# Kernel tuning notes

Measured on AMD Instinct MI355X. Metric: run time of the kernel, lower is better.

The kernel has to match this reference:

```python
import jax, jax.numpy as jnp
import numpy as np
import math

B, T, D = 4, 2048, 1024
H, KD, VD = 16, 64, 64


def setup_inputs() -> dict:
    key = jax.random.key(0)
    ks = jax.random.split(key, 10)
    s = 1.0 / math.sqrt(D)
    x = jax.random.normal(ks[0], (B, T, D), dtype=jnp.float32)
    # causal mask: True above the diagonal (positions to be masked out)
    mask = jnp.triu(jnp.ones((1, T, T), dtype=bool), k=1)
    Wq = jax.random.normal(ks[1], (H * KD, D), dtype=jnp.float32) * s
    bq = jnp.zeros((H * KD,), dtype=jnp.float32)
    Wk = jax.random.normal(ks[2], (H * KD, D), dtype=jnp.float32) * s
    bk = jnp.zeros((H * KD,), dtype=jnp.float32)
    Wv = jax.random.normal(ks[3], (H * VD, D), dtype=jnp.float32) * s
    bv = jnp.zeros((H * VD,), dtype=jnp.float32)
    Wo = jax.random.normal(ks[4], (D, H * VD), dtype=jnp.float32) * (1.0 / math.sqrt(H * VD))
    bo = jnp.zeros((D,), dtype=jnp.float32)
    return {"x": x, "mask": mask, "Wq": Wq, "bq": bq, "Wk": Wk, "bk": bk,
            "Wv": Wv, "bv": bv, "Wo": Wo, "bo": bo}


def reference(x, mask, Wq, bq, Wk, bk, Wv, bv, Wo, bo):
    b, t, d = x.shape
    # projections, reshaped to (b, h, t, head_dim)
    q = (x @ Wq.T + bq).reshape(b, t, H, KD).transpose(0, 2, 1, 3)
    k = (x @ Wk.T + bk).reshape(b, t, H, KD).transpose(0, 2, 1, 3)
    v = (x @ Wv.T + bv).reshape(b, t, H, VD).transpose(0, 2, 1, 3)
    scores = jnp.einsum('bhqd,bhkd->bhqk', q, k) / jnp.sqrt(jnp.float32(KD))
    # mask [1,T,T] broadcasts over batch and heads
    scores = jnp.where(mask[:, None, :, :], -jnp.inf, scores)
    attn = jax.nn.softmax(scores, axis=-1)
    out = jnp.einsum('bhqk,bhkd->bhqd', attn, v)  # (b,h,t,vd)
    out = out.transpose(0, 2, 1, 3).reshape(b, t, H * VD)
    return out @ Wo.T + bo
```

## Files before the change

### kernel.cpp

```cpp
#include <hip/hip_runtime.h>
#include <hip/hip_bf16.h>
#include <stdint.h>

#define B_ 4
#define T_ 2048
#define D_ 1024
#define H_ 16
#define HD_ 64

typedef __attribute__((ext_vector_type(8))) short bf16x8;
typedef __attribute__((ext_vector_type(4))) float f32x4;
typedef __attribute__((ext_vector_type(16))) float f32x16;

static __device__ __forceinline__ short f2bf(float f) {
    __hip_bfloat16 h = __float2bfloat16(f);
    short s;
    __builtin_memcpy(&s, &h, sizeof(short));
    return s;
}
static __device__ __forceinline__ float bf2f(short s) {
    unsigned u = ((unsigned)(unsigned short)s) << 16;
    float f;
    __builtin_memcpy(&f, &u, sizeof(float));
    return f;
}

static __device__ __forceinline__ void gload16(const void* g, void* l) {
    __builtin_amdgcn_global_load_lds((const __attribute__((address_space(1))) uint32_t*)g,
                                     (__attribute__((address_space(3))) uint32_t*)l,
                                     16, 0, 0);
}

static __device__ __forceinline__ unsigned cvtpk(float lo, float hi) {
    unsigned r;
    asm("v_cvt_pk_bf16_f32 %0, %1, %2" : "=v"(r) : "v"(lo), "v"(hi));
    return r;
}
static __device__ __forceinline__ void pl32swap(unsigned& a, unsigned& b) {
    asm("v_permlane32_swap_b32 %0, %1" : "+v"(a), "+v"(b));
}

__global__ __launch_bounds__(256) void cast_kernel(const float* __restrict__ src,
                                                   short* __restrict__ dst, int n) {
    int i = (blockIdx.x * 256 + threadIdx.x) * 4;
    if (i < n) {
        float4 v = *reinterpret_cast<const float4*>(src + i);
        short4 o;
        o.x = f2bf(v.x); o.y = f2bf(v.y); o.z = f2bf(v.z); o.w = f2bf(v.w);
        *reinterpret_cast<short4*>(dst + i) = o;
    }
}

__global__ __launch_bounds__(256) void cast_w_kernel(const float* __restrict__ wq,
                                                     const float* __restrict__ wk,
                                                     const float* __restrict__ wv,
                                                     const float* __restrict__ wo,
                                                     short* __restrict__ wqkv,
                                                     short* __restrict__ wob) {
    int wsel = blockIdx.x >> 10;
    int blk = blockIdx.x & 1023;
    const float* src = wsel == 0 ? wq : (wsel == 1 ? wk : (wsel == 2 ? wv : wo));
    short* dst = wsel == 3 ? wob : (wqkv + (size_t)wsel * 1024 * 1024);
    int i = (blk * 256 + threadIdx.x) * 4;
    float4 v = *reinterpret_cast<const float4*>(src + i);
    short4 o;
    o.x = f2bf(v.x); o.y = f2bf(v.y); o.z = f2bf(v.z); o.w = f2bf(v.w);
    *reinterpret_cast<short4*>(dst + i) = o;
}

template <int MODE>
__global__ __launch_bounds__(256) void gemm_kernel(
        const short* __restrict__ A, const short* __restrict__ Bw,
        const float* __restrict__ b0, const float* __restrict__ b1, const float* __restrict__ b2,
        short* __restrict__ q_out, short* __restrict__ k_out, short* __restrict__ v_out,
        float* __restrict__ f_out) {
    const int K = 1024;
    const int n0 = blockIdx.x * 128;
    const int m0 = blockIdx.y * 128;
    const int tid = threadIdx.x;
    const int wid = tid >> 6, lane = tid & 63, g = lane >> 4, c = lane & 15;
    const int wr = wid >> 1, wc = wid & 1;

    __shared__ __align__(16) short As[128 * 32];
    __shared__ __align__(16) short Bs[128 * 32];

    f32x4 acc[4][4] = {};

    for (int k0 = 0; k0 < K; k0 += 32) {
        #pragma unroll
        for (int r = 0; r < 2; ++r) {
            int ci = r * 256 + tid;
            int row = ci >> 2, cc = ci & 3;
            gload16(A + (size_t)(m0 + row) * K + k0 + cc * 8, As + ci * 8);
            gload16(Bw + (size_t)(n0 + row) * K + k0 + cc * 8, Bs + ci * 8);
        }
        __syncthreads();
        bf16x8 af[4], bfr[4];
        #pragma unroll
        for (int mt = 0; mt < 4; ++mt)
            af[mt] = *reinterpret_cast<const bf16x8*>(As + (wr * 64 + mt * 16 + c) * 32 + g * 8);
        #pragma unroll
        for (int nt = 0; nt < 4; ++nt)
            bfr[nt] = *reinterpret_cast<const bf16x8*>(Bs + (wc * 64 + nt * 16 + c) * 32 + g * 8);
        #pragma unroll
        for (int mt = 0; mt < 4; ++mt) {
            #pragma unroll
            for (int nt = 0; nt < 4; ++nt)
                acc[mt][nt] = __builtin_amdgcn_mfma_f32_16x16x32_bf16(af[mt], bfr[nt], acc[mt][nt], 0, 0, 0);
        }
        __syncthreads();
    }

    #pragma unroll
    for (int mt = 0; mt < 4; ++mt) {
        #pragma unroll
        for (int nt = 0; nt < 4; ++nt) {
            int n = n0 + wc * 64 + nt * 16 + c;
            if (MODE == 0) {
                int part = n >> 10, n1 = n & 1023;
                const float* bias = part == 0 ? b0 : (part == 1 ? b1 : b2);
                short* op = part == 0 ? q_out : (part == 1 ? k_out : v_out);
                int h = n1 >> 6, d = n1 & 63;
                float bb = bias[n1];
                #pragma unroll
                for (int r = 0; r < 4; ++r) {
                    int m = m0 + wr * 64 + mt * 16 + g * 4 + r;
                    int b = m >> 11, t = m & (T_ - 1);
                    op[((size_t)(b * H_ + h) * T_ + t) * HD_ + d] = f2bf(acc[mt][nt][r] + bb);
                }
            } else {
                float bb = b0[n];
                #pragma unroll
                for (int r = 0; r < 4; ++r) {
                    int m = m0 + wr * 64 + mt * 16 + g * 4 + r;
                    f_out[(size_t)m * 1024 + n] = acc[mt][nt][r] + bb;
                }
            }
        }
    }
}

__global__ __launch_bounds__(256) void attn_kernel(const short* __restrict__ q,
                                                   const short* __restrict__ k,
                                                   const short* __restrict__ v,
                                                   short* __restrict__ o,
                                                   short* __restrict__ pO,
                                                   float* __restrict__ pml) {
    const int h = blockIdx.y, b = blockIdx.z;
    const size_t base = ((size_t)(b * H_ + h)) * T_ * HD_;
    const int tid = threadIdx.x;
    const int wid = tid >> 6, lane = tid & 63;
    const int ql = lane & 31, hi = lane >> 5;
    const int xr = (ql & 7) << 3;

    const int bxx = blockIdx.x;
    const int grp = bxx / 3, r3 = bxx - grp * 3;
    int j, t_begin, t_end, s = 0;
    bool partial;
    if (r3 < 2) { partial = true;  j = 15 - grp; s = r3; t_begin = s * (j + 1); t_end = t_begin + (j + 1); }
    else        { partial = false; j = 7 - grp;  t_begin = 0; t_end = 2 * j + 2; }

    const int q0b = j * 128;
    const int q0w = q0b + wid * 32;
    const int qg = q0w + ql;

    __shared__ __align__(16) short lds[16384];

    const int krr = tid >> 3, ksl = tid & 7;
    const int vkey = tid & 63, vd0b = tid >> 6;

    bf16x8 qf[4];
    {
        const short* qrow = q + base + (size_t)qg * HD_ + hi * 8;
        #pragma unroll
        for (int st = 0; st < 4; ++st)
            qf[st] = *reinterpret_cast<const bf16x8*>(qrow + st * 16);
    }

    f32x16 oT0 = {}, oT1 = {};
    float m_r = -1e30f, l_r = 0.f;

    {
        const int kv0 = t_begin * 64;
        #pragma unroll
        for (int r = 0; r < 2; ++r) {
            int row = r * 32 + krr;
            gload16(k + base + (size_t)(kv0 + row) * HD_ + ((ksl ^ (row & 7)) << 3),
                    lds + r * 2048 + tid * 8);
        }
        #pragma unroll
        for (int cc = 0; cc < 2; ++cc) {
            int vd0 = vd0b + cc * 4;
            bf16x8 vv = *reinterpret_cast<const bf16x8*>(v + base + (size_t)(kv0 + vkey) * HD_ + vd0 * 8);
            #pragma unroll
            for (int jx = 0; jx < 8; ++jx)
                lds[8192 + (vd0 * 8 + jx) * 64 + (vkey ^ (jx << 3))] = vv[jx];
        }
    }
    __syncthreads();

    int buf = 0;
    for (int t0 = t_begin; t0 < t_end; ++t0) {
        const int kv0 = t0 * 64;
        const bool pf = (t0 + 1 < t_end);
        bf16x8 vnext[2];
        if (pf) {
            #pragma unroll
            for (int r = 0; r < 2; ++r) {
                int row = r * 32 + krr;
                gload16(k + base + (size_t)(kv0 + 64 + row) * HD_ + ((ksl ^ (row & 7)) << 3),
                        lds + (buf ^ 1) * 4096 + r * 2048 + tid * 8);
            }
            #pragma unroll
            for (int cc = 0; cc < 2; ++cc)
                vnext[cc] = *reinterpret_cast<const bf16x8*>(
                    v + base + (size_t)(kv0 + 64 + vkey) * HD_ + (vd0b + cc * 4) * 8);
        }

        if (kv0 <= q0w + 31) {
            const short* Kb = lds + buf * 4096;
            const short* Vb = lds + 8192 + buf * 4096;

            f32x16 s0 = {}, s1 = {};
            __builtin_amdgcn_s_setprio(1);
            #pragma unroll
            for (int st = 0; st < 4; ++st) {
                int coff = (st * 16 + hi * 8) ^ xr;
                bf16x8 ka0 = *reinterpret_cast<const bf16x8*>(Kb + ql * 64 + coff);
                bf16x8 ka1 = *reinterpret_cast<const bf16x8*>(Kb + (32 + ql) * 64 + coff);
                s0 = __builtin_amdgcn_mfma_f32_32x32x16_bf16(ka0, qf[st], s0, 0, 0, 0);
                s1 = __builtin_amdgcn_mfma_f32_32x32x16_bf16(ka1, qf[st], s1, 0, 0, 0);
            }
            __builtin_amdgcn_s_setprio(0);

            const float SC = 0.18033688f;
            if (kv0 + 63 <= q0w) {
                #pragma unroll
                for (int i = 0; i < 16; ++i) { s0[i] *= SC; s1[i] *= SC; }
            } else {
                #pragma unroll
                for (int i = 0; i < 16; ++i) {
                    int krow = (i & 3) + 8 * (i >> 2) + 4 * hi;
                    s0[i] = (kv0 + krow > qg) ? -1e30f : s0[i] * SC;
                    s1[i] = (kv0 + 32 + krow > qg) ? -1e30f : s1[i] * SC;
                }
            }

            float t8[8], t4[4], t2[2], tm;
            {
                f32x16 mx;
                #pragma unroll
                for (int i = 0; i < 16; ++i) mx[i] = fmaxf(s0[i], s1[i]);
                #pragma unroll
                for (int i = 0; i < 8; ++i) t8[i] = fmaxf(mx[i], mx[i + 8]);
                #pragma unroll
                for (int i = 0; i < 4; ++i) t4[i] = fmaxf(t8[i], t8[i + 4]);
                t2[0] = fmaxf(t4[0], t4[2]); t2[1] = fmaxf(t4[1], t4[3]);
                tm = fmaxf(t2[0], t2[1]);
            }
            tm = fmaxf(tm, __shfl_xor(tm, 32, 64));

            if (!__all(tm <= m_r + 8.f)) {
                float mn = fmaxf(m_r, tm);
                float al = exp2f(m_r - mn);
                m_r = mn;
                l_r *= al;
                #pragma unroll
                for (int i = 0; i < 16; ++i) { oT0[i] *= al; oT1[i] *= al; }
            }

            #pragma unroll
            for (int i = 0; i < 16; ++i) s0[i] = exp2f(s0[i] - m_r);
            #pragma unroll
            for (int i = 0; i < 16; ++i) s1[i] = exp2f(s1[i] - m_r);

            {
                f32x16 sv = s0 + s1;
                #pragma unroll
                for (int i = 0; i < 8; ++i) t8[i] = sv[i] + sv[i + 8];
                #pragma unroll
                for (int i = 0; i < 4; ++i) t4[i] = t8[i] + t8[i + 4];
                t2[0] = t4[0] + t4[2]; t2[1] = t4[1] + t4[3];
                float ts = t2[0] + t2[1];
                ts += __shfl_xor(ts, 32, 64);
                l_r += ts;
            }

            unsigned c[16];
            #pragma unroll
            for (int i = 0; i < 8; ++i) c[i] = cvtpk(s0[2 * i], s0[2 * i + 1]);
            #pragma unroll
            for (int i = 0; i < 8; ++i) c[8 + i] = cvtpk(s1[2 * i], s1[2 * i + 1]);
            pl32swap(c[0], c[2]);   pl32swap(c[1], c[3]);
            pl32swap(c[4], c[6]);   pl32swap(c[5], c[7]);
            pl32swap(c[8], c[10]);  pl32swap(c[9], c[11]);
            pl32swap(c[12], c[14]); pl32swap(c[13], c[15]);
            union { unsigned u[4]; bf16x8 v8; } pb[4];
            #pragma unroll
            for (int ksx = 0; ksx < 4; ++ksx) {
                #pragma unroll
                for (int jx = 0; jx < 4; ++jx) pb[ksx].u[jx] = c[ksx * 4 + jx];
            }

            __builtin_amdgcn_s_setprio(1);
            #pragma unroll
            for (int ksx = 0; ksx < 4; ++ksx) {
                int coff = (ksx * 16 + hi * 8) ^ xr;
                bf16x8 va0 = *reinterpret_cast<const bf16x8*>(Vb + ql * 64 + coff);
                bf16x8 va1 = *reinterpret_cast<const bf16x8*>(Vb + (32 + ql) * 64 + coff);
                oT0 = __builtin_amdgcn_mfma_f32_32x32x16_bf16(va0, pb[ksx].v8, oT0, 0, 0, 0);
                oT1 = __builtin_amdgcn_mfma_f32_32x32x16_bf16(va1, pb[ksx].v8, oT1, 0, 0, 0);
            }
            __builtin_amdgcn_s_setprio(0);
        }

        if (pf) {
            #pragma unroll
            for (int cc = 0; cc < 2; ++cc) {
                int vd0 = vd0b + cc * 4;
                #pragma unroll
                for (int jx = 0; jx < 8; ++jx)
                    lds[8192 + (buf ^ 1) * 4096 + (vd0 * 8 + jx) * 64 + (vkey ^ (jx << 3))] = vnext[cc][jx];
            }
        }
        __syncthreads();
        buf ^= 1;
    }

    float inv = 1.f / l_r;
    const int row = wid * 32 + ql;
    #pragma unroll
    for (int i = 0; i < 16; ++i) {
        int d0 = (i & 3) + 8 * (i >> 2) + 4 * hi;
        lds[8192 + row * 64 + (d0 ^ xr)] = f2bf(oT0[i] * inv);
        lds[8192 + row * 64 + ((d0 + 32) ^ xr)] = f2bf(oT1[i] * inv);
    }
    if (partial && hi == 0) {
        size_t prow = ((((size_t)(b * H_ + h)) * 8 + (j - 8)) * 2 + s) * 128 + row;
        *reinterpret_cast<float2*>(pml + prow * 2) = make_float2(m_r, l_r);
    }
    __syncthreads();
    if (partial) {
        size_t prow0 = ((((size_t)(b * H_ + h)) * 8 + (j - 8)) * 2 + s) * 128;
        #pragma unroll
        for (int rr = 0; rr < 4; ++rr) {
            int orow = rr * 32 + (tid >> 3);
            int sl = tid & 7;
            bf16x8 val = *reinterpret_cast<const bf16x8*>(lds + 8192 + orow * 64 + ((sl ^ (orow & 7)) << 3));
            *reinterpret_cast<bf16x8*>(pO + (prow0 + orow) * 64 + sl * 8) = val;
        }
    } else {
        #pragma unroll
        for (int rr = 0; rr < 4; ++rr) {
            int orow = rr * 32 + (tid >> 3);
            int sl = tid & 7;
            bf16x8 val = *reinterpret_cast<const bf16x8*>(lds + 8192 + orow * 64 + ((sl ^ (orow & 7)) << 3));
            *reinterpret_cast<bf16x8*>(o + ((size_t)(b * T_ + q0b + orow)) * D_ + h * HD_ + sl * 8) = val;
        }
    }
}

__global__ __launch_bounds__(256) void merge_kernel(const short* __restrict__ pO,
                                                    const float* __restrict__ pml,
                                                    short* __restrict__ ab) {
    int gid = blockIdx.x * 256 + threadIdx.x;
    int d8 = gid & 7;
    int r  = (gid >> 3) & 127;
    int jj = (gid >> 10) & 7;
    int bh = gid >> 13;
    int b = bh >> 4, h = bh & 15;
    size_t prow0 = (((size_t)bh * 8 + jj) * 2) * 128;
    float m0 = pml[(prow0 + r) * 2],       l0 = pml[(prow0 + r) * 2 + 1];
    float m1 = pml[(prow0 + 128 + r) * 2], l1 = pml[(prow0 + 128 + r) * 2 + 1];
    float M = fmaxf(m0, m1);
    float w0 = exp2f(m0 - M) * l0, w1 = exp2f(m1 - M) * l1;
    float inv = 1.f / (w0 + w1);
    w0 *= inv; w1 *= inv;
    bf16x8 a = *reinterpret_cast<const bf16x8*>(pO + (prow0 + r) * 64 + d8 * 8);
    bf16x8 c = *reinterpret_cast<const bf16x8*>(pO + (prow0 + 128 + r) * 64 + d8 * 8);
    short res[8];
    #pragma unroll
    for (int i = 0; i < 8; ++i) res[i] = f2bf(w0 * bf2f(a[i]) + w1 * bf2f(c[i]));
    int t = (jj + 8) * 128 + r;
    *reinterpret_cast<bf16x8*>(ab + ((size_t)(b * T_ + t)) * D_ + h * HD_ + d8 * 8) =
        *reinterpret_cast<const bf16x8*>(res);
}

extern "C" void kernel_launch(void* const* d_in, const int* in_sizes, int n_in,
                              void* d_out, int out_size, void* d_ws, size_t ws_size,
                              hipStream_t stream) {
    const float* x  = (const float*)d_in[0];
    const float* Wq = (const float*)d_in[2];
    const float* bq = (const float*)d_in[3];
    const float* Wk = (const float*)d_in[4];
    const float* bk = (const float*)d_in[5];
    const float* Wv = (const float*)d_in[6];
    const float* bv = (const float*)d_in[7];
    const float* Wo = (const float*)d_in[8];
    const float* bo = (const float*)d_in[9];
    float* out = (float*)d_out;

    const size_t NX = (size_t)B_ * T_ * D_;
    const size_t NW = (size_t)D_ * D_;

    short* ws   = (short*)d_ws;
    short* xb   = ws;
    short* ab   = ws;
    short* wqkv = xb + NX;
    short* wob  = wqkv + 3 * NW;
    short* qb   = wob + NW;
    short* kb   = qb + NX;
    short* vb   = kb + NX;
    short* pO   = (short*)d_out;
    float* pml  = (float*)((short*)d_out + (size_t)64 * 8 * 2 * 128 * 64);

    cast_kernel<<<(int)(NX / 1024), 256, 0, stream>>>(x, xb, (int)NX);
    cast_w_kernel<<<4096, 256, 0, stream>>>(Wq, Wk, Wv, Wo, wqkv, wob);

    gemm_kernel<0><<<dim3(24, 64), 256, 0, stream>>>(xb, wqkv, bq, bk, bv, qb, kb, vb, nullptr);
    attn_kernel<<<dim3(24, H_, B_), 256, 0, stream>>>(qb, kb, vb, ab, pO, pml);
    merge_kernel<<<2048, 256, 0, stream>>>(pO, pml, ab);
    gemm_kernel<1><<<dim3(8, 64), 256, 0, stream>>>(ab, wob, bo, nullptr, nullptr, nullptr,
                                                    nullptr, nullptr, out);
}
```

Measured before the change: 332.8 us.

## Use 256-row attention blocks with 512 threads and deepen GEMM K-tile

The attention kernel now uses 512-thread blocks that each cover 256 query rows, so every 64-key K/V tile loaded into LDS is shared by eight waves instead of four. The causal work split is rebalanced with a lookup table of 12 blocks per head, and the partial-result layout and merge kernel are changed to match. The output staging reuses the K buffer region of LDS. Separately, the projection GEMM now loads a 64-wide K slice per iteration, halving the number of barriers, at the cost of twice the shared memory per block.

```diff
diff --git a/kernel.cpp b/kernel.cpp
--- a/kernel.cpp
+++ b/kernel.cpp
@@ -81,32 +81,35 @@
     const int wid = tid >> 6, lane = tid & 63, g = lane >> 4, c = lane & 15;
     const int wr = wid >> 1, wc = wid & 1;
 
-    __shared__ __align__(16) short As[128 * 32];
-    __shared__ __align__(16) short Bs[128 * 32];
+    __shared__ __align__(16) short As[128 * 64];
+    __shared__ __align__(16) short Bs[128 * 64];
 
     f32x4 acc[4][4] = {};
 
-    for (int k0 = 0; k0 < K; k0 += 32) {
-        #pragma unroll
-        for (int r = 0; r < 2; ++r) {
+    for (int k0 = 0; k0 < K; k0 += 64) {
+        #pragma unroll
+        for (int r = 0; r < 4; ++r) {
             int ci = r * 256 + tid;
-            int row = ci >> 2, cc = ci & 3;
+            int row = ci >> 3, cc = ci & 7;
             gload16(A + (size_t)(m0 + row) * K + k0 + cc * 8, As + ci * 8);
             gload16(Bw + (size_t)(n0 + row) * K + k0 + cc * 8, Bs + ci * 8);
         }
         __syncthreads();
-        bf16x8 af[4], bfr[4];
-        #pragma unroll
-        for (int mt = 0; mt < 4; ++mt)
-            af[mt] = *reinterpret_cast<const bf16x8*>(As + (wr * 64 + mt * 16 + c) * 32 + g * 8);
-        #pragma unroll
-        for (int nt = 0; nt < 4; ++nt)
-            bfr[nt] = *reinterpret_cast<const bf16x8*>(Bs + (wc * 64 + nt * 16 + c) * 32 + g * 8);
-        #pragma unroll
-        for (int mt = 0; mt < 4; ++mt) {
+        #pragma unroll
+        for (int ks = 0; ks < 2; ++ks) {
+            bf16x8 af[4], bfr[4];
+            #pragma unroll
+            for (int mt = 0; mt < 4; ++mt)
+                af[mt] = *reinterpret_cast<const bf16x8*>(As + (wr * 64 + mt * 16 + c) * 64 + ks * 32 + g * 8);
             #pragma unroll
             for (int nt = 0; nt < 4; ++nt)
-                acc[mt][nt] = __builtin_amdgcn_mfma_f32_16x16x32_bf16(af[mt], bfr[nt], acc[mt][nt], 0, 0, 0);
+                bfr[nt] = *reinterpret_cast<const bf16x8*>(Bs + (wc * 64 + nt * 16 + c) * 64 + ks * 32 + g * 8);
+            #pragma unroll
+            for (int mt = 0; mt < 4; ++mt) {
+                #pragma unroll
+                for (int nt = 0; nt < 4; ++nt)
+                    acc[mt][nt] = __builtin_amdgcn_mfma_f32_16x16x32_bf16(af[mt], bfr[nt], acc[mt][nt], 0, 0, 0);
+            }
         }
         __syncthreads();
     }
@@ -140,7 +143,7 @@
     }
 }
 
-__global__ __launch_bounds__(256) void attn_kernel(const short* __restrict__ q,
+__global__ __launch_bounds__(512) void attn_kernel(const short* __restrict__ q,
                                                    const short* __restrict__ k,
                                                    const short* __restrict__ v,
                                                    short* __restrict__ o,
@@ -153,21 +156,24 @@
     const int ql = lane & 31, hi = lane >> 5;
     const int xr = (ql & 7) << 3;
 
+    const int jt[12] = {7, 7, 3, 6, 6, 5, 5, 2, 4, 4, 1, 0};
+    const int stt[12] = {0, 1, 0, 0, 1, 0, 1, 0, 0, 1, 0, 0};
+    const int ptt[12] = {1, 1, 0, 1, 1, 1, 1, 0, 1, 1, 0, 0};
     const int bxx = blockIdx.x;
-    const int grp = bxx / 3, r3 = bxx - grp * 3;
-    int j, t_begin, t_end, s = 0;
-    bool partial;
-    if (r3 < 2) { partial = true;  j = 15 - grp; s = r3; t_begin = s * (j + 1); t_end = t_begin + (j + 1); }
-    else        { partial = false; j = 7 - grp;  t_begin = 0; t_end = 2 * j + 2; }
-
-    const int q0b = j * 128;
+    const int j2 = jt[bxx], s = stt[bxx];
+    const bool partial = ptt[bxx] != 0;
+    int t_begin, t_end;
+    if (partial) { t_begin = s * (2 * j2 + 2); t_end = t_begin + 2 * j2 + 2; }
+    else         { t_begin = 0;               t_end = 4 * j2 + 4; }
+
+    const int q0b = j2 * 256;
     const int q0w = q0b + wid * 32;
     const int qg = q0w + ql;
 
     __shared__ __align__(16) short lds[16384];
 
     const int krr = tid >> 3, ksl = tid & 7;
-    const int vkey = tid & 63, vd0b = tid >> 6;
+    const int vkey = tid & 63, vd0 = tid >> 6;
 
     bf16x8 qf[4];
     {
@@ -182,20 +188,11 @@
 
     {
         const int kv0 = t_begin * 64;
-        #pragma unroll
-        for (int r = 0; r < 2; ++r) {
-            int row = r * 32 + krr;
-            gload16(k + base + (size_t)(kv0 + row) * HD_ + ((ksl ^ (row & 7)) << 3),
-                    lds + r * 2048 + tid * 8);
-        }
-        #pragma unroll
-        for (int cc = 0; cc < 2; ++cc) {
-            int vd0 = vd0b + cc * 4;
-            bf16x8 vv = *reinterpret_cast<const bf16x8*>(v + base + (size_t)(kv0 + vkey) * HD_ + vd0 * 8);
-            #pragma unroll
-            for (int jx = 0; jx < 8; ++jx)
-                lds[8192 + (vd0 * 8 + jx) * 64 + (vkey ^ (jx << 3))] = vv[jx];
-        }
+        gload16(k + base + (size_t)(kv0 + krr) * HD_ + ((ksl ^ (krr & 7)) << 3), lds + tid * 8);
+        bf16x8 vv = *reinterpret_cast<const bf16x8*>(v + base + (size_t)(kv0 + vkey) * HD_ + vd0 * 8);
+        #pragma unroll
+        for (int jx = 0; jx < 8; ++jx)
+            lds[8192 + (vd0 * 8 + jx) * 64 + (vkey ^ (jx << 3))] = vv[jx];
     }
     __syncthreads();
 
@@ -203,18 +200,11 @@
     for (int t0 = t_begin; t0 < t_end; ++t0) {
         const int kv0 = t0 * 64;
         const bool pf = (t0 + 1 < t_end);
-        bf16x8 vnext[2];
+        bf16x8 vnext;
         if (pf) {
-            #pragma unroll
-            for (int r = 0; r < 2; ++r) {
-                int row = r * 32 + krr;
-                gload16(k + base + (size_t)(kv0 + 64 + row) * HD_ + ((ksl ^ (row & 7)) << 3),
-                        lds + (buf ^ 1) * 4096 + r * 2048 + tid * 8);
-            }
-            #pragma unroll
-            for (int cc = 0; cc < 2; ++cc)
-                vnext[cc] = *reinterpret_cast<const bf16x8*>(
-                    v + base + (size_t)(kv0 + 64 + vkey) * HD_ + (vd0b + cc * 4) * 8);
+            gload16(k + base + (size_t)(kv0 + 64 + krr) * HD_ + ((ksl ^ (krr & 7)) << 3),
+                    lds + (buf ^ 1) * 4096 + tid * 8);
+            vnext = *reinterpret_cast<const bf16x8*>(v + base + (size_t)(kv0 + 64 + vkey) * HD_ + vd0 * 8);
         }
 
         if (kv0 <= q0w + 31) {
@@ -316,12 +306,8 @@
 
         if (pf) {
             #pragma unroll
-            for (int cc = 0; cc < 2; ++cc) {
-                int vd0 = vd0b + cc * 4;
-                #pragma unroll
-                for (int jx = 0; jx < 8; ++jx)
-                    lds[8192 + (buf ^ 1) * 4096 + (vd0 * 8 + jx) * 64 + (vkey ^ (jx << 3))] = vnext[cc][jx];
-            }
+            for (int jx = 0; jx < 8; ++jx)
+                lds[8192 + (buf ^ 1) * 4096 + (vd0 * 8 + jx) * 64 + (vkey ^ (jx << 3))] = vnext[jx];
         }
         __syncthreads();
         buf ^= 1;
@@ -332,29 +318,29 @@
     #pragma unroll
     for (int i = 0; i < 16; ++i) {
         int d0 = (i & 3) + 8 * (i >> 2) + 4 * hi;
-        lds[8192 + row * 64 + (d0 ^ xr)] = f2bf(oT0[i] * inv);
-        lds[8192 + row * 64 + ((d0 + 32) ^ xr)] = f2bf(oT1[i] * inv);
+        lds[row * 64 + (d0 ^ xr)] = f2bf(oT0[i] * inv);
+        lds[row * 64 + ((d0 + 32) ^ xr)] = f2bf(oT1[i] * inv);
     }
     if (partial && hi == 0) {
-        size_t prow = ((((size_t)(b * H_ + h)) * 8 + (j - 8)) * 2 + s) * 128 + row;
+        size_t prow = ((((size_t)(b * H_ + h)) * 4 + (j2 - 4)) * 2 + s) * 256 + row;
         *reinterpret_cast<float2*>(pml + prow * 2) = make_float2(m_r, l_r);
     }
     __syncthreads();
     if (partial) {
-        size_t prow0 = ((((size_t)(b * H_ + h)) * 8 + (j - 8)) * 2 + s) * 128;
+        size_t prow0 = ((((size_t)(b * H_ + h)) * 4 + (j2 - 4)) * 2 + s) * 256;
         #pragma unroll
         for (int rr = 0; rr < 4; ++rr) {
-            int orow = rr * 32 + (tid >> 3);
+            int orow = rr * 64 + (tid >> 3);
             int sl = tid & 7;
-            bf16x8 val = *reinterpret_cast<const bf16x8*>(lds + 8192 + orow * 64 + ((sl ^ (orow & 7)) << 3));
+            bf16x8 val = *reinterpret_cast<const bf16x8*>(lds + orow * 64 + ((sl ^ (orow & 7)) << 3));
             *reinterpret_cast<bf16x8*>(pO + (prow0 + orow) * 64 + sl * 8) = val;
         }
     } else {
         #pragma unroll
         for (int rr = 0; rr < 4; ++rr) {
-            int orow = rr * 32 + (tid >> 3);
+            int orow = rr * 64 + (tid >> 3);
             int sl = tid & 7;
-            bf16x8 val = *reinterpret_cast<const bf16x8*>(lds + 8192 + orow * 64 + ((sl ^ (orow & 7)) << 3));
+            bf16x8 val = *reinterpret_cast<const bf16x8*>(lds + orow * 64 + ((sl ^ (orow & 7)) << 3));
             *reinterpret_cast<bf16x8*>(o + ((size_t)(b * T_ + q0b + orow)) * D_ + h * HD_ + sl * 8) = val;
         }
     }
@@ -365,23 +351,23 @@
                                                     short* __restrict__ ab) {
     int gid = blockIdx.x * 256 + threadIdx.x;
     int d8 = gid & 7;
-    int r  = (gid >> 3) & 127;
-    int jj = (gid >> 10) & 7;
+    int r  = (gid >> 3) & 255;
+    int jj = (gid >> 11) & 3;
     int bh = gid >> 13;
     int b = bh >> 4, h = bh & 15;
-    size_t prow0 = (((size_t)bh * 8 + jj) * 2) * 128;
+    size_t prow0 = (((size_t)bh * 4 + jj) * 2) * 256;
     float m0 = pml[(prow0 + r) * 2],       l0 = pml[(prow0 + r) * 2 + 1];
-    float m1 = pml[(prow0 + 128 + r) * 2], l1 = pml[(prow0 + 128 + r) * 2 + 1];
+    float m1 = pml[(prow0 + 256 + r) * 2], l1 = pml[(prow0 + 256 + r) * 2 + 1];
     float M = fmaxf(m0, m1);
     float w0 = exp2f(m0 - M) * l0, w1 = exp2f(m1 - M) * l1;
     float inv = 1.f / (w0 + w1);
     w0 *= inv; w1 *= inv;
     bf16x8 a = *reinterpret_cast<const bf16x8*>(pO + (prow0 + r) * 64 + d8 * 8);
-    bf16x8 c = *reinterpret_cast<const bf16x8*>(pO + (prow0 + 128 + r) * 64 + d8 * 8);
+    bf16x8 c = *reinterpret_cast<const bf16x8*>(pO + (prow0 + 256 + r) * 64 + d8 * 8);
     short res[8];
     #pragma unroll
     for (int i = 0; i < 8; ++i) res[i] = f2bf(w0 * bf2f(a[i]) + w1 * bf2f(c[i]));
-    int t = (jj + 8) * 128 + r;
+    int t = (jj + 4) * 256 + r;
     *reinterpret_cast<bf16x8*>(ab + ((size_t)(b * T_ + t)) * D_ + h * HD_ + d8 * 8) =
         *reinterpret_cast<const bf16x8*>(res);
 }
@@ -412,13 +398,13 @@
     short* kb   = qb + NX;
     short* vb   = kb + NX;
     short* pO   = (short*)d_out;
-    float* pml  = (float*)((short*)d_out + (size_t)64 * 8 * 2 * 128 * 64);
+    float* pml  = (float*)((short*)d_out + (size_t)64 * 4 * 2 * 256 * 64);
 
     cast_kernel<<<(int)(NX / 1024), 256, 0, stream>>>(x, xb, (int)NX);
     cast_w_kernel<<<4096, 256, 0, stream>>>(Wq, Wk, Wv, Wo, wqkv, wob);
 
     gemm_kernel<0><<<dim3(24, 64), 256, 0, stream>>>(xb, wqkv, bq, bk, bv, qb, kb, vb, nullptr);
-    attn_kernel<<<dim3(24, H_, B_), 256, 0, stream>>>(qb, kb, vb, ab, pO, pml);
+    attn_kernel<<<dim3(12, H_, B_), 512, 0, stream>>>(qb, kb, vb, ab, pO, pml);
     merge_kernel<<<2048, 256, 0, stream>>>(pO, pml, ab);
     gemm_kernel<1><<<dim3(8, 64), 256, 0, stream>>>(ab, wob, bo, nullptr, nullptr, nullptr,
                                                     nullptr, nullptr, out);
```

New measurement: 347.4 us. 4.4% more time.

## Triple-buffer K tiles with two-ahead prefetch and manual waitcnt barriers

Applied to the files above, without the earlier changes.

The attention kernel now keeps K in three LDS buffers and prefetches K two tiles ahead with direct global-to-LDS loads, while V stays double-buffered through registers. The per-iteration __syncthreads is replaced by explicit s_waitcnt vmcnt counts plus s_barrier, with sched_barriers fixing instruction order. The goal is to hide more global-load latency behind the MFMA work. In exchange, LDS use per block grows, which may lower occupancy, and the hand-counted vmcnt values must exactly match the number of loads in flight or the kernel can read stale data.

```diff
diff --git a/kernel.cpp b/kernel.cpp
--- a/kernel.cpp
+++ b/kernel.cpp
@@ -164,7 +164,7 @@
     const int q0w = q0b + wid * 32;
     const int qg = q0w + ql;
 
-    __shared__ __align__(16) short lds[16384];
+    __shared__ __align__(16) short lds[20480];
 
     const int krr = tid >> 3, ksl = tid & 7;
     const int vkey = tid & 63, vd0b = tid >> 6;
@@ -180,46 +180,71 @@
     f32x16 oT0 = {}, oT1 = {};
     float m_r = -1e30f, l_r = 0.f;
 
+    int kcur = 0, knx = 1, knx2 = 2, vcur = 0;
+
     {
         const int kv0 = t_begin * 64;
+        bf16x8 vv[2];
+        #pragma unroll
+        for (int cc = 0; cc < 2; ++cc)
+            vv[cc] = *reinterpret_cast<const bf16x8*>(v + base + (size_t)(kv0 + vkey) * HD_ + (vd0b + cc * 4) * 8);
+        __builtin_amdgcn_sched_barrier(0);
         #pragma unroll
         for (int r = 0; r < 2; ++r) {
             int row = r * 32 + krr;
             gload16(k + base + (size_t)(kv0 + row) * HD_ + ((ksl ^ (row & 7)) << 3),
                     lds + r * 2048 + tid * 8);
         }
-        #pragma unroll
-        for (int cc = 0; cc < 2; ++cc) {
-            int vd0 = vd0b + cc * 4;
-            bf16x8 vv = *reinterpret_cast<const bf16x8*>(v + base + (size_t)(kv0 + vkey) * HD_ + vd0 * 8);
-            #pragma unroll
-            for (int jx = 0; jx < 8; ++jx)
-                lds[8192 + (vd0 * 8 + jx) * 64 + (vkey ^ (jx << 3))] = vv[jx];
-        }
-    }
-    __syncthreads();
-
-    int buf = 0;
-    for (int t0 = t_begin; t0 < t_end; ++t0) {
-        const int kv0 = t0 * 64;
-        const bool pf = (t0 + 1 < t_end);
-        bf16x8 vnext[2];
-        if (pf) {
+        if (t_begin + 1 < t_end) {
             #pragma unroll
             for (int r = 0; r < 2; ++r) {
                 int row = r * 32 + krr;
                 gload16(k + base + (size_t)(kv0 + 64 + row) * HD_ + ((ksl ^ (row & 7)) << 3),
-                        lds + (buf ^ 1) * 4096 + r * 2048 + tid * 8);
-            }
+                        lds + 4096 + r * 2048 + tid * 8);
+            }
+        }
+        __builtin_amdgcn_sched_barrier(0);
+        #pragma unroll
+        for (int cc = 0; cc < 2; ++cc) {
+            int vd0 = vd0b + cc * 4;
+            #pragma unroll
+            for (int jx = 0; jx < 8; ++jx)
+                lds[12288 + (vd0 * 8 + jx) * 64 + (vkey ^ (jx << 3))] = vv[cc][jx];
+        }
+        if (t_begin + 1 < t_end)
+            asm volatile("s_waitcnt vmcnt(2) lgkmcnt(0)" ::: "memory");
+        else
+            asm volatile("s_waitcnt vmcnt(0) lgkmcnt(0)" ::: "memory");
+        __builtin_amdgcn_s_barrier();
+        __builtin_amdgcn_sched_barrier(0);
+    }
+
+    for (int t0 = t_begin; t0 < t_end; ++t0) {
+        const int kv0 = t0 * 64;
+        const bool pf1 = (t0 + 1 < t_end);
+        const bool pf2 = (t0 + 2 < t_end);
+
+        bf16x8 vn[2];
+        if (pf1) {
             #pragma unroll
             for (int cc = 0; cc < 2; ++cc)
-                vnext[cc] = *reinterpret_cast<const bf16x8*>(
+                vn[cc] = *reinterpret_cast<const bf16x8*>(
                     v + base + (size_t)(kv0 + 64 + vkey) * HD_ + (vd0b + cc * 4) * 8);
         }
+        __builtin_amdgcn_sched_barrier(0);
+        if (pf2) {
+            #pragma unroll
+            for (int r = 0; r < 2; ++r) {
+                int row = r * 32 + krr;
+                gload16(k + base + (size_t)(kv0 + 128 + row) * HD_ + ((ksl ^ (row & 7)) << 3),
+                        lds + knx2 * 4096 + r * 2048 + tid * 8);
+            }
+        }
+        __builtin_amdgcn_sched_barrier(0);
 
         if (kv0 <= q0w + 31) {
-            const short* Kb = lds + buf * 4096;
-            const short* Vb = lds + 8192 + buf * 4096;
+            const short* Kb = lds + kcur * 4096;
+            const short* Vb = lds + 12288 + vcur * 4096;
 
             f32x16 s0 = {}, s1 = {};
             __builtin_amdgcn_s_setprio(1);
@@ -314,26 +339,34 @@
             __builtin_amdgcn_s_setprio(0);
         }
 
-        if (pf) {
+        if (pf1) {
             #pragma unroll
             for (int cc = 0; cc < 2; ++cc) {
                 int vd0 = vd0b + cc * 4;
                 #pragma unroll
                 for (int jx = 0; jx < 8; ++jx)
-                    lds[8192 + (buf ^ 1) * 4096 + (vd0 * 8 + jx) * 64 + (vkey ^ (jx << 3))] = vnext[cc][jx];
-            }
-        }
-        __syncthreads();
-        buf ^= 1;
-    }
+                    lds[12288 + (vcur ^ 1) * 4096 + (vd0 * 8 + jx) * 64 + (vkey ^ (jx << 3))] = vn[cc][jx];
+            }
+            if (pf2)
+                asm volatile("s_waitcnt vmcnt(2) lgkmcnt(0)" ::: "memory");
+            else
+                asm volatile("s_waitcnt vmcnt(0) lgkmcnt(0)" ::: "memory");
+            __builtin_amdgcn_s_barrier();
+            __builtin_amdgcn_sched_barrier(0);
+        }
+
+        int tmpk = kcur; kcur = knx; knx = knx2; knx2 = tmpk;
+        vcur ^= 1;
+    }
+    __syncthreads();
 
     float inv = 1.f / l_r;
     const int row = wid * 32 + ql;
     #pragma unroll
     for (int i = 0; i < 16; ++i) {
         int d0 = (i & 3) + 8 * (i >> 2) + 4 * hi;
-        lds[8192 + row * 64 + (d0 ^ xr)] = f2bf(oT0[i] * inv);
-        lds[8192 + row * 64 + ((d0 + 32) ^ xr)] = f2bf(oT1[i] * inv);
+        lds[12288 + row * 64 + (d0 ^ xr)] = f2bf(oT0[i] * inv);
+        lds[12288 + row * 64 + ((d0 + 32) ^ xr)] = f2bf(oT1[i] * inv);
     }
     if (partial && hi == 0) {
         size_t prow = ((((size_t)(b * H_ + h)) * 8 + (j - 8)) * 2 + s) * 128 + row;
@@ -346,7 +379,7 @@
         for (int rr = 0; rr < 4; ++rr) {
             int orow = rr * 32 + (tid >> 3);
             int sl = tid & 7;
-            bf16x8 val = *reinterpret_cast<const bf16x8*>(lds + 8192 + orow * 64 + ((sl ^ (orow & 7)) << 3));
+            bf16x8 val = *reinterpret_cast<const bf16x8*>(lds + 12288 + orow * 64 + ((sl ^ (orow & 7)) << 3));
             *reinterpret_cast<bf16x8*>(pO + (prow0 + orow) * 64 + sl * 8) = val;
         }
     } else {
@@ -354,7 +387,7 @@
         for (int rr = 0; rr < 4; ++rr) {
             int orow = rr * 32 + (tid >> 3);
             int sl = tid & 7;
-            bf16x8 val = *reinterpret_cast<const bf16x8*>(lds + 8192 + orow * 64 + ((sl ^ (orow & 7)) << 3));
+            bf16x8 val = *reinterpret_cast<const bf16x8*>(lds + 12288 + orow * 64 + ((sl ^ (orow & 7)) << 3));
             *reinterpret_cast<bf16x8*>(o + ((size_t)(b * T_ + q0b + orow)) * D_ + h * HD_ + sl * 8) = val;
         }
     }
```

After: 322.3 us. -3.2%, faster.
